# Kernel optimization log

Hardware: AMD Instinct MI355X
Metric: run time of the kernel (lower is better)

The kernel has to match this reference:

```python
import jax, jax.numpy as jnp
import numpy as np

MAX_DISP = 4  # init kwarg maxDisplacement


def setup_inputs() -> dict:
    key = jax.random.key(0)
    k1, k2 = jax.random.split(key)
    F1 = jax.random.normal(k1, (8, 128, 128, 128), dtype=jnp.float32)
    F2 = jax.random.normal(k2, (8, 128, 128, 128), dtype=jnp.float32)
    return {"F1": F1, "F2": F2}


def reference(F1, F2):
    d = MAX_DISP
    B, H, W, C = F1.shape
    # Zero-pad F2 spatially by d on each side (NHWC)
    padded = jnp.pad(F2, ((0, 0), (d, d), (d, d), (0, 0)))
    max_offset = 2 * d + 1
    # For each (dy, dx) shift: channel-mean of F1 * shifted-F2 -> [B,H,W]
    costs = [
        jnp.mean(F1 * padded[:, y:y + H, x:x + W, :], axis=3)
        for y in range(max_offset)
        for x in range(max_offset)
    ]
    cost_volume = jnp.stack(costs, axis=3)  # [B, H, W, max_offset^2]
    return jax.nn.leaky_relu(cost_volume, negative_slope=0.1)
```

## Files before the change

### kernel.cpp

```cpp
#include <hip/hip_runtime.h>
#include <hip/hip_bf16.h>
#include <string.h>

typedef __attribute__((ext_vector_type(8))) short bf16x8;
typedef __attribute__((ext_vector_type(4))) float f32x4;

namespace {
constexpr int B = 8, H = 128, W = 128, C = 128;
constexpr int MO = 9, NOFF = 81;
constexpr int ROWS = 4;
constexpr int WCOLS = 16;
constexpr int F2R = 12;
constexpr int SREAL = 24;
constexpr int NT = 512;
constexpr int TOT = 2304;
constexpr int NLD = 5;
constexpr int KSTR = SREAL * 32;
constexpr int ROWSTR = 4 * KSTR;
constexpr int PADS = 256;
}

__device__ inline unsigned bf2pack(float a, float b) {
  __hip_bfloat162 h = __float22bfloat162_rn(float2{a, b});
  unsigned r;
  memcpy(&r, &h, sizeof(r));
  return r;
}

__device__ __forceinline__ f32x4 mfma16(bf16x8 a, bf16x8 b, f32x4 c) {
  return __builtin_amdgcn_mfma_f32_16x16x32_bf16(a, b, c, 0, 0, 0);
}

__global__ __launch_bounds__(NT, 4) void costvol_kernel(
    const float* __restrict__ F1, const float* __restrict__ F2,
    float* __restrict__ out)
{
  __shared__ __align__(16) short sF2[F2R * ROWSTR + PADS];

  const int lin  = blockIdx.x;
  const int b    = lin & 7;
  const int tile = lin >> 3;
  const int rt   = tile & 31;
  const int wt   = tile >> 5;
  const int h0   = rt * ROWS;
  const int wb0  = wt * WCOLS;

  const int tid  = threadIdx.x;
  const int wv   = tid >> 6;
  const int r    = wv >> 1;
  const int hh   = wv & 1;
  const int lane = tid & 63;
  const int j    = lane & 15;
  const int kq   = lane >> 4;

  int gofs[NLD]; int lofs[NLD]; unsigned okm = 0; unsigned act = 0;
#pragma unroll
  for (int it = 0; it < NLD; ++it) {
    const int idx = tid + it * NT;
    if (idx < TOT) {
      act |= 1u << it;
      const int kg   = idx & 7;
      const int slot = idx >> 3;
      const int ry   = slot / SREAL;
      const int s    = slot - ry * SREAL;
      const int fy   = h0 - 4 + ry;
      const int fx   = wb0 - 4 + s;
      const bool ok  = ((unsigned)fy < 128u) && ((unsigned)fx < 128u);
      okm |= (unsigned)ok << it;
      gofs[it] = ok ? (((b * H + fy) * W + fx) * C + kg * 4) : 0;
      lofs[it] = ry * ROWSTR + s * 32 + kg * 4;
    } else {
      gofs[it] = 0; lofs[it] = 0;
    }
  }

  auto issue = [&](int g, float4* ld) {
#pragma unroll
    for (int it = 0; it < NLD; ++it) {
      if ((act >> it) & 1u) {
        ld[it] = *reinterpret_cast<const float4*>(F2 + gofs[it] + g * 32);
      }
    }
    __builtin_amdgcn_sched_barrier(0);
  };
  auto pack = [&](int g, const float4* ld) {
#pragma unroll
    for (int it = 0; it < NLD; ++it) {
      if (((act & okm) >> it) & 1u) {
        uint2 p;
        p.x = bf2pack(ld[it].x, ld[it].y);
        p.y = bf2pack(ld[it].z, ld[it].w);
        *reinterpret_cast<uint2*>(&sF2[lofs[it] + g * KSTR]) = p;
      }
    }
  };

  float4 ldA[NLD], ldB[NLD];
  issue(0, ldA);
  issue(1, ldB);
#pragma unroll
  for (int it = 0; it < NLD; ++it) {
    if (((act & ~okm) >> it) & 1u) {
#pragma unroll
      for (int g = 0; g < 4; ++g) {
        *reinterpret_cast<uint2*>(&sF2[lofs[it] + g * KSTR]) = uint2{0u, 0u};
      }
    }
  }
  pack(0, ldA);
  issue(2, ldA);
  pack(1, ldB);
  issue(3, ldB);
  pack(2, ldA);

  const float* f1p = F1 + (((size_t)b * H + h0 + r) * W + wb0 + j) * C + kq * 8;
  float4 u0[4], u1[4];
#pragma unroll
  for (int kk = 0; kk < 4; ++kk) {
    u0[kk] = *reinterpret_cast<const float4*>(f1p + kk * 32);
    u1[kk] = *reinterpret_cast<const float4*>(f1p + kk * 32 + 4);
  }
  __builtin_amdgcn_sched_barrier(0);
  pack(3, ldB);

  bf16x8 afrag[4];
  constexpr float S = 0.0078125f;
#pragma unroll
  for (int kk = 0; kk < 4; ++kk) {
    uint4 q;
    q.x = bf2pack(u0[kk].x * S, u0[kk].y * S);
    q.y = bf2pack(u0[kk].z * S, u0[kk].w * S);
    q.z = bf2pack(u1[kk].x * S, u1[kk].y * S);
    q.w = bf2pack(u1[kk].z * S, u1[kk].w * S);
    afrag[kk] = __builtin_bit_cast(bf16x8, q);
  }

  __syncthreads();

  f32x4 acc[5][2];
#pragma unroll
  for (int s = 0; s < 5; ++s) { acc[s][0] = {0,0,0,0}; acc[s][1] = {0,0,0,0}; }

  const int rybase = r + hh * 4;
  const short* bb = sF2 + j * 32 + kq * 8;
  __builtin_amdgcn_s_setprio(1);
#pragma unroll
  for (int kk = 0; kk < 4; ++kk) {
    const short* bk = bb + kk * KSTR;
#pragma unroll
    for (int s = 0; s < 5; ++s) {
      const short* brow = bk + (rybase + s) * ROWSTR;
      const bf16x8 b0 = *reinterpret_cast<const bf16x8*>(brow);
      const bf16x8 b1 = *reinterpret_cast<const bf16x8*>(brow + 512);
      acc[s][0] = mfma16(afrag[kk], b0, acc[s][0]);
      acc[s][1] = mfma16(afrag[kk], b1, acc[s][1]);
    }
  }
  __builtin_amdgcn_s_setprio(0);

  float* lb = out + (((size_t)b * H + h0 + r) * W + wb0) * NOFF +
              kq * 320 + j + hh * 36;
#pragma unroll
  for (int t = 0; t < 2; ++t) {
#pragma unroll
    for (int reg = 0; reg < 4; ++reg) {
      const int dxl = j + 16 * t - kq * 4 - reg;
      if ((unsigned)dxl <= 8u) {
#pragma unroll
        for (int s = 0; s < 5; ++s) {
          float m = acc[s][t][reg];
          m = fmaxf(m, 0.1f * m);
          lb[reg * 80 + 16 * t + s * 9] = m;
        }
      }
    }
  }
}

extern "C" void kernel_launch(void* const* d_in, const int* in_sizes, int n_in,
                              void* d_out, int out_size, void* d_ws, size_t ws_size,
                              hipStream_t stream) {
  const float* F1 = (const float*)d_in[0];
  const float* F2 = (const float*)d_in[1];
  float* out = (float*)d_out;
  dim3 grid(B * (H / ROWS) * (W / WCOLS));
  dim3 block(NT);
  hipLaunchKernelGGL(costvol_kernel, grid, block, 0, stream, F1, F2, out);
}
```

Measured before the change: 51.15 us.

## Load F2 operands directly from global memory instead of staging in LDS

Drops the shared-memory staging of the padded F2 tile, along with the barrier and the cooperative load/pack pipeline. Each wave now reads its B fragments straight from global memory (out-of-bounds rows and columns point at a zeroed workspace buffer) and converts them to bf16 in registers before each MFMA. This removes LDS traffic and the synchronisation point, but each F2 element is now re-read many times across waves and offsets, and converted redundantly. It also adds a memset launch and lowers the occupancy hint from 4 to 3.

Result: slower. 165.0 us (+222.6%).

```diff
diff --git a/kernel.cpp b/kernel.cpp
--- a/kernel.cpp
+++ b/kernel.cpp
@@ -7,17 +7,10 @@
 
 namespace {
 constexpr int B = 8, H = 128, W = 128, C = 128;
-constexpr int MO = 9, NOFF = 81;
+constexpr int NOFF = 81;
 constexpr int ROWS = 4;
 constexpr int WCOLS = 16;
-constexpr int F2R = 12;
-constexpr int SREAL = 24;
 constexpr int NT = 512;
-constexpr int TOT = 2304;
-constexpr int NLD = 5;
-constexpr int KSTR = SREAL * 32;
-constexpr int ROWSTR = 4 * KSTR;
-constexpr int PADS = 256;
 }
 
 __device__ inline unsigned bf2pack(float a, float b) {
@@ -31,12 +24,10 @@
   return __builtin_amdgcn_mfma_f32_16x16x32_bf16(a, b, c, 0, 0, 0);
 }
 
-__global__ __launch_bounds__(NT, 4) void costvol_kernel(
+__global__ __launch_bounds__(NT, 3) void costvol_kernel(
     const float* __restrict__ F1, const float* __restrict__ F2,
-    float* __restrict__ out)
+    const float* __restrict__ zpad, float* __restrict__ out)
 {
-  __shared__ __align__(16) short sF2[F2R * ROWSTR + PADS];
-
   const int lin  = blockIdx.x;
   const int b    = lin & 7;
   const int tile = lin >> 3;
@@ -53,66 +44,6 @@
   const int j    = lane & 15;
   const int kq   = lane >> 4;
 
-  int gofs[NLD]; int lofs[NLD]; unsigned okm = 0; unsigned act = 0;
-#pragma unroll
-  for (int it = 0; it < NLD; ++it) {
-    const int idx = tid + it * NT;
-    if (idx < TOT) {
-      act |= 1u << it;
-      const int kg   = idx & 7;
-      const int slot = idx >> 3;
-      const int ry   = slot / SREAL;
-      const int s    = slot - ry * SREAL;
-      const int fy   = h0 - 4 + ry;
-      const int fx   = wb0 - 4 + s;
-      const bool ok  = ((unsigned)fy < 128u) && ((unsigned)fx < 128u);
-      okm |= (unsigned)ok << it;
-      gofs[it] = ok ? (((b * H + fy) * W + fx) * C + kg * 4) : 0;
-      lofs[it] = ry * ROWSTR + s * 32 + kg * 4;
-    } else {
-      gofs[it] = 0; lofs[it] = 0;
-    }
-  }
-
-  auto issue = [&](int g, float4* ld) {
-#pragma unroll
-    for (int it = 0; it < NLD; ++it) {
-      if ((act >> it) & 1u) {
-        ld[it] = *reinterpret_cast<const float4*>(F2 + gofs[it] + g * 32);
-      }
-    }
-    __builtin_amdgcn_sched_barrier(0);
-  };
-  auto pack = [&](int g, const float4* ld) {
-#pragma unroll
-    for (int it = 0; it < NLD; ++it) {
-      if (((act & okm) >> it) & 1u) {
-        uint2 p;
-        p.x = bf2pack(ld[it].x, ld[it].y);
-        p.y = bf2pack(ld[it].z, ld[it].w);
-        *reinterpret_cast<uint2*>(&sF2[lofs[it] + g * KSTR]) = p;
-      }
-    }
-  };
-
-  float4 ldA[NLD], ldB[NLD];
-  issue(0, ldA);
-  issue(1, ldB);
-#pragma unroll
-  for (int it = 0; it < NLD; ++it) {
-    if (((act & ~okm) >> it) & 1u) {
-#pragma unroll
-      for (int g = 0; g < 4; ++g) {
-        *reinterpret_cast<uint2*>(&sF2[lofs[it] + g * KSTR]) = uint2{0u, 0u};
-      }
-    }
-  }
-  pack(0, ldA);
-  issue(2, ldA);
-  pack(1, ldB);
-  issue(3, ldB);
-  pack(2, ldA);
-
   const float* f1p = F1 + (((size_t)b * H + h0 + r) * W + wb0 + j) * C + kq * 8;
   float4 u0[4], u1[4];
 #pragma unroll
@@ -120,8 +51,19 @@
     u0[kk] = *reinterpret_cast<const float4*>(f1p + kk * 32);
     u1[kk] = *reinterpret_cast<const float4*>(f1p + kk * 32 + 4);
   }
-  __builtin_amdgcn_sched_barrier(0);
-  pack(3, ldB);
+
+  const float* pB[5][2];
+  const int rybase = r + hh * 4;
+#pragma unroll
+  for (int s = 0; s < 5; ++s) {
+    const int fy = h0 - 4 + rybase + s;
+#pragma unroll
+    for (int t = 0; t < 2; ++t) {
+      const int fx = wb0 - 4 + j + 16 * t;
+      const bool ok = ((unsigned)fy < 128u) && ((unsigned)fx < 128u);
+      pB[s][t] = ok ? (F2 + (((size_t)b * H + fy) * W + fx) * C) : zpad;
+    }
+  }
 
   bf16x8 afrag[4];
   constexpr float S = 0.0078125f;
@@ -135,28 +77,29 @@
     afrag[kk] = __builtin_bit_cast(bf16x8, q);
   }
 
-  __syncthreads();
-
   f32x4 acc[5][2];
 #pragma unroll
   for (int s = 0; s < 5; ++s) { acc[s][0] = {0,0,0,0}; acc[s][1] = {0,0,0,0}; }
 
-  const int rybase = r + hh * 4;
-  const short* bb = sF2 + j * 32 + kq * 8;
-  __builtin_amdgcn_s_setprio(1);
 #pragma unroll
   for (int kk = 0; kk < 4; ++kk) {
-    const short* bk = bb + kk * KSTR;
 #pragma unroll
     for (int s = 0; s < 5; ++s) {
-      const short* brow = bk + (rybase + s) * ROWSTR;
-      const bf16x8 b0 = *reinterpret_cast<const bf16x8*>(brow);
-      const bf16x8 b1 = *reinterpret_cast<const bf16x8*>(brow + 512);
-      acc[s][0] = mfma16(afrag[kk], b0, acc[s][0]);
-      acc[s][1] = mfma16(afrag[kk], b1, acc[s][1]);
+      const float* p0 = pB[s][0] + kk * 32 + kq * 8;
+      const float* p1 = pB[s][1] + kk * 32 + kq * 8;
+      const float4 x0 = *reinterpret_cast<const float4*>(p0);
+      const float4 x1 = *reinterpret_cast<const float4*>(p0 + 4);
+      const float4 y0 = *reinterpret_cast<const float4*>(p1);
+      const float4 y1 = *reinterpret_cast<const float4*>(p1 + 4);
+      uint4 q0, q1;
+      q0.x = bf2pack(x0.x, x0.y); q0.y = bf2pack(x0.z, x0.w);
+      q0.z = bf2pack(x1.x, x1.y); q0.w = bf2pack(x1.z, x1.w);
+      q1.x = bf2pack(y0.x, y0.y); q1.y = bf2pack(y0.z, y0.w);
+      q1.z = bf2pack(y1.x, y1.y); q1.w = bf2pack(y1.z, y1.w);
+      acc[s][0] = mfma16(afrag[kk], __builtin_bit_cast(bf16x8, q0), acc[s][0]);
+      acc[s][1] = mfma16(afrag[kk], __builtin_bit_cast(bf16x8, q1), acc[s][1]);
     }
   }
-  __builtin_amdgcn_s_setprio(0);
 
   float* lb = out + (((size_t)b * H + h0 + r) * W + wb0) * NOFF +
               kq * 320 + j + hh * 36;
@@ -183,7 +126,9 @@
   const float* F1 = (const float*)d_in[0];
   const float* F2 = (const float*)d_in[1];
   float* out = (float*)d_out;
+  hipMemsetAsync(d_ws, 0, 1024, stream);
+  const float* zpad = (const float*)d_ws;
   dim3 grid(B * (H / ROWS) * (W / WCOLS));
   dim3 block(NT);
-  hipLaunchKernelGGL(costvol_kernel, grid, block, 0, stream, F1, F2, out);
+  hipLaunchKernelGGL(costvol_kernel, grid, block, 0, stream, F1, F2, zpad, out);
 }
```
